# Kernel optimization log

Hardware: AMD Instinct MI355X
Metric: run time of the kernel (lower is better)

Reference implementation:

```python
import jax, jax.numpy as jnp
import numpy as np

MAX_NUM_CENTERS = 100
CENTER_IGNORE_PX = 3
SIGMA = 2.0   # center_gt_blur
KSIZE = 21    # GaussianLayer kernel size (ReflectionPad2d(10) + Conv2d(k=21))


def _gauss_kernel():
    r = KSIZE // 2
    x = jnp.arange(-r, r + 1, dtype=jnp.float32)
    g = jnp.exp(-0.5 * (x / SIGMA) ** 2)
    g = g / g.sum()
    return jnp.outer(g, g)  # [21,21], sums to 1 (matches scipy gaussian_filter of a delta)


def _gaussian_blur(x):
    # x: [B,H,W] -> depthwise 21x21 gaussian with reflect padding (GaussianLayer)
    r = KSIZE // 2
    k = _gauss_kernel()[None, None]  # [1,1,21,21]
    xp = jnp.pad(x[:, None], ((0, 0), (0, 0), (r, r), (r, r)), mode="reflect")
    y = jax.lax.conv_general_dilated(xp, k, (1, 1), "VALID",
                                     dimension_numbers=("NCHW", "OIHW", "NCHW"))
    return y[:, 0]


def setup_inputs() -> dict:
    key = jax.random.key(0)
    k1, k2 = jax.random.split(key)
    B, H, W = 8, 768, 768
    instances = jax.random.randint(k1, (B, 1, H, W), 0, MAX_NUM_CENTERS, dtype=jnp.int32)
    centers = jax.random.uniform(k2, (B, MAX_NUM_CENTERS, 2), dtype=jnp.float32) * (H - 1) + 1.0
    return {"instances": instances, "centers": centers}


def reference(instances, centers):
    B, _, H, W = instances.shape
    inst = instances[:, 0]                                # [B,H,W]
    col = jnp.arange(W, dtype=jnp.float32)                # xym_s[0][i,j] = j
    row = jnp.arange(H, dtype=jnp.float32)[:, None]       # xym_s[1][i,j] = i

    valid = inst > 0                                      # instance_mask
    has_inst = jnp.any(valid, axis=(1, 2)).astype(jnp.float32)  # len(unique)>1 gate

    # per-pixel nearest-center gather: center = centers[b, id-1]
    idx = jnp.clip(inst - 1, 0, MAX_NUM_CENTERS - 1)
    c = centers[jnp.arange(B)[:, None, None], idx]        # [B,H,W,2]
    gt_cx = jnp.where(valid, c[..., 1], -10000.0)         # gt_center_x (swapped coords)
    gt_cy = jnp.where(valid, c[..., 0], -10000.0)

    gt_X = gt_cx - row                                    # gt_center_x - xym_s[1]
    gt_Y = gt_cy - col                                    # gt_center_y - xym_s[0]

    near = (jnp.abs(gt_X) < CENTER_IGNORE_PX) & (jnp.abs(gt_Y) < CENTER_IGNORE_PX)
    # batches with no instances skip the block -> ignore stays all-ones
    ignore = jnp.where(has_inst[:, None, None] > 0, (~near).astype(jnp.float32), 1.0)

    m = valid.astype(jnp.float32)
    R = jnp.sqrt(gt_X ** 2 + gt_Y ** 2) * m
    theta_raw = jnp.arctan2(gt_Y, gt_X)
    theta = theta_raw * has_inst[:, None, None]           # skipped (zero) when no instances
    s = jnp.sin(theta_raw) * m
    cth = jnp.cos(theta_raw) * m
    M = jnp.sqrt(s ** 2 + cth ** 2)                       # == m, kept for faithfulness
    s = jnp.where(valid, s / jnp.maximum(M, 1e-12), 0.0)
    cth = jnp.where(valid, cth / jnp.maximum(M, 1e-12), 0.0)

    # gt_center_mask: zeros if no center-neighborhood pixels, else normalized blur
    blur = _gaussian_blur(1.0 - ignore)
    all_ones = jnp.all(ignore >= 1.0, axis=(1, 2))        # gt_center_mask.all()
    bmax = jnp.max(blur, axis=(1, 2), keepdims=True)
    cmask = jnp.where(all_ones[:, None, None], 0.0, blur / jnp.maximum(bmax, 1e-12))

    top = jnp.stack([R, theta, s, cth, ignore, cmask], axis=1)       # [B,6,H,W]
    mat = jnp.concatenate([top, jnp.zeros((B, 7, H, W), top.dtype)], axis=1)[:, :, None]
    # mat: [B,13,1,H,W]; channels 6..12 are zero (no orientation input)

    # gt_centers[id] = centers[b, id-1][[1,0]] for each instance id present
    present = jnp.zeros((B, MAX_NUM_CENTERS), dtype=bool).at[
        jnp.arange(B)[:, None], inst.reshape(B, -1)].set(True)
    swapped = centers[..., ::-1]
    gt_centers = jnp.zeros_like(centers).at[:, 1:, :].set(
        jnp.where(present[:, 1:, None], swapped[:, :-1, :], 0.0))

    return mat, gt_centers
```

## Files before the change

kernel.cpp:

```cpp
#include <hip/hip_runtime.h>
#include <math.h>

#define NB 8
#define NH 768
#define NW 768
#define NHW (NH*NW)
#define NCEN 100
#define NPIX (NB*NHW)
#define RAD 10
#define KS 21

#define TS 64
#define HALO 10
#define MS (TS + 2*HALO)
#define TILES_X (NW / TS)
#define TILES_PER_B (TILES_X * TILES_X)
#define SCAN_BLKS (NPIX / 4096)
#define BLKS_PER_B (NHW / 4096)

#define HDR_HAS 32
#define HDR_NEAR 40
#define HDR_BMAX 48
#define HDR_BLOCKMASK 64

typedef float f4 __attribute__((ext_vector_type(4)));

__device__ __forceinline__ int refl(int i, int n) {
    i = i < 0 ? -i : i;
    return i >= n ? 2 * n - 2 - i : i;
}

__global__ void k_scan(const int4* __restrict__ inst4, int* __restrict__ hdr) {
    __shared__ unsigned sm[4];
    int t = threadIdx.x;
    if (t < 4) sm[t] = 0;
    __syncthreads();
    unsigned m0 = 0, m1 = 0, m2 = 0, m3 = 0;
    size_t base = (size_t)blockIdx.x * 1024 + t;
#pragma unroll
    for (int q = 0; q < 4; q++) {
        int4 v = inst4[base + (size_t)q * 256];
        int a[4] = {v.x, v.y, v.z, v.w};
#pragma unroll
        for (int e = 0; e < 4; e++) {
            int iv = a[e];
            if (iv > 0) {
                unsigned bit = 1u << (iv & 31);
                int w = iv >> 5;
                if (w == 0) m0 |= bit; else if (w == 1) m1 |= bit;
                else if (w == 2) m2 |= bit; else m3 |= bit;
            }
        }
    }
#pragma unroll
    for (int off = 32; off >= 1; off >>= 1) {
        m0 |= __shfl_xor(m0, off);
        m1 |= __shfl_xor(m1, off);
        m2 |= __shfl_xor(m2, off);
        m3 |= __shfl_xor(m3, off);
    }
    if ((t & 63) == 0) {
        if (m0) atomicOr(&sm[0], m0);
        if (m1) atomicOr(&sm[1], m1);
        if (m2) atomicOr(&sm[2], m2);
        if (m3) atomicOr(&sm[3], m3);
    }
    __syncthreads();
    if (t < 4) ((unsigned*)&hdr[HDR_BLOCKMASK])[blockIdx.x * 4 + t] = sm[t];
}

__global__ void k_small(const float* __restrict__ centers, int* __restrict__ hdr,
                        float* __restrict__ gt) {
    __shared__ unsigned s_pres[32];
    int t = threadIdx.x;
    const unsigned* bm = (const unsigned*)&hdr[HDR_BLOCKMASK];
    if (t < 32) {
        int b = t >> 2, wi = t & 3;
        unsigned acc = 0;
        for (int k = 0; k < BLKS_PER_B; k++) acc |= bm[(b * BLKS_PER_B + k) * 4 + wi];
        s_pres[t] = acc;
    }
    if (t >= 40 && t < 56) hdr[t] = 0;
    __syncthreads();
    if (t < NB * NCEN) {
        int b = t / NCEN, k = t - b * NCEN;
        float vx = 0.f, vy = 0.f;
        if (k >= 1) {
            unsigned w = s_pres[b * 4 + (k >> 5)];
            if ((w >> (k & 31)) & 1u) {
                vx = centers[(b * NCEN + (k - 1)) * 2 + 1];
                vy = centers[(b * NCEN + (k - 1)) * 2 + 0];
            }
        }
        gt[t * 2 + 0] = vx;
        gt[t * 2 + 1] = vy;
    } else if (t < NB * NCEN + NB) {
        int b = t - NB * NCEN;
        unsigned any = (s_pres[b * 4] & 0xFFFFFFFEu)
                     | s_pres[b * 4 + 1] | s_pres[b * 4 + 2] | s_pres[b * 4 + 3];
        hdr[HDR_HAS + b] = any ? 1 : 0;
    }
}

__global__ __launch_bounds__(256) void k_fused(const int* __restrict__ inst,
                                               const float* __restrict__ centers,
                                               int* __restrict__ hdr,
                                               float* __restrict__ out) {
    __shared__ float s_cen[2 * NCEN];
    __shared__ float s_mask[MS * MS];
    __shared__ float s_hbuf[MS * TS];
    __shared__ float s_w[KS];
    __shared__ float s_red[4];

    int t = threadIdx.x;
    int tile = blockIdx.x;
    int b = tile / TILES_PER_B;
    int tr = tile - b * TILES_PER_B;
    int ti0 = (tr / TILES_X) * TS;
    int tj0 = (tr - (tr / TILES_X) * TILES_X) * TS;

    if (t == 0) {
        float v[KS];
        float sum = 0.f;
        for (int k = 0; k < KS; k++) {
            float x = (float)(k - RAD) * 0.5f;
            v[k] = expf(-0.5f * x * x);
            sum += v[k];
        }
        for (int k = 0; k < KS; k++) s_w[k] = v[k] / sum;
    }
    for (int k = t; k < 2 * NCEN; k += 256) s_cen[k] = centers[b * 2 * NCEN + k];
    int has = hdr[HDR_HAS + b];
    __syncthreads();

    int anynear = 0;
    const int* instb = inst + (size_t)b * NHW;
    for (int e = t; e < MS * MS; e += 256) {
        int r = e / MS, c = e - r * MS;
        int gi = refl(ti0 + r - HALO, NH);
        int gj = refl(tj0 + c - HALO, NW);
        int iv = instb[gi * NW + gj];
        float mv = 0.f;
        if (has && iv > 0) {
            int idx = iv - 1;
            float cy = s_cen[2 * idx];
            float cx = s_cen[2 * idx + 1];
            float X = cx - (float)gi;
            float Y = cy - (float)gj;
            if (fabsf(X) < 3.f && fabsf(Y) < 3.f) { mv = 1.f; anynear = 1; }
        }
        s_mask[e] = mv;
    }
    if (anynear) hdr[HDR_NEAR + b] = 1;
    __syncthreads();

    for (int e = t; e < MS * TS; e += 256) {
        int r = e >> 6, c = e & 63;
        const float* mrow = &s_mask[r * MS + c];
        float acc = 0.f;
#pragma unroll
        for (int k = 0; k < KS; k++) acc += s_w[k] * mrow[k];
        s_hbuf[e] = acc;
    }
    __syncthreads();

    float wmax = 0.f;
    float* outb = out + (size_t)b * 13 * NHW;
    for (int q = t; q < TS * TS / 4; q += 256) {
        int r = q >> 4;
        int c0 = (q & 15) * 4;
        f4 blur = {0.f, 0.f, 0.f, 0.f};
#pragma unroll
        for (int k = 0; k < KS; k++) {
            f4 hv = *(const f4*)&s_hbuf[(r + k) * TS + c0];
            blur += s_w[k] * hv;
        }
        wmax = fmaxf(wmax, fmaxf(fmaxf(blur.x, blur.y), fmaxf(blur.z, blur.w)));

        int gi = ti0 + r, gj0 = tj0 + c0;
        int p0 = gi * NW + gj0;
        int4 ivv = *(const int4*)&instb[p0];
        int ia[4] = {ivv.x, ivv.y, ivv.z, ivv.w};
        f4 vR, vTh, vS, vC, vIg;
#pragma unroll
        for (int e = 0; e < 4; e++) {
            int iv = ia[e];
            bool valid = iv > 0;
            int idx = iv - 1;
            idx = idx < 0 ? 0 : idx;
            float cy = s_cen[2 * idx];
            float cx = s_cen[2 * idx + 1];
            float gcx = valid ? cx : -10000.f;
            float gcy = valid ? cy : -10000.f;
            float X = gcx - (float)gi;
            float Y = gcy - (float)(gj0 + e);
            bool near = (fabsf(X) < 3.f) && (fabsf(Y) < 3.f);
            vIg[e] = (has != 0) ? (near ? 0.f : 1.f) : 1.f;
            float m = valid ? 1.f : 0.f;
            float R2 = X * X + Y * Y;
            vR[e] = sqrtf(R2) * m;
            float rinv = R2 > 0.f ? rsqrtf(R2) : 0.f;
            vS[e] = valid ? Y * rinv : 0.f;
            vC[e] = valid ? (R2 > 0.f ? X * rinv : 1.f) : 0.f;
            float th = atan2f(Y, X);
            vTh[e] = (has != 0) ? th : 0.f;
        }
        __builtin_nontemporal_store(vR,   (f4*)&outb[(size_t)0 * NHW + p0]);
        __builtin_nontemporal_store(vTh,  (f4*)&outb[(size_t)1 * NHW + p0]);
        __builtin_nontemporal_store(vS,   (f4*)&outb[(size_t)2 * NHW + p0]);
        __builtin_nontemporal_store(vC,   (f4*)&outb[(size_t)3 * NHW + p0]);
        __builtin_nontemporal_store(vIg,  (f4*)&outb[(size_t)4 * NHW + p0]);
        __builtin_nontemporal_store(blur, (f4*)&outb[(size_t)5 * NHW + p0]);
        f4 z = {0.f, 0.f, 0.f, 0.f};
#pragma unroll
        for (int ch = 6; ch < 13; ++ch)
            __builtin_nontemporal_store(z, (f4*)&outb[(size_t)ch * NHW + p0]);
    }

#pragma unroll
    for (int off = 32; off >= 1; off >>= 1) wmax = fmaxf(wmax, __shfl_down(wmax, off));
    if ((t & 63) == 0) s_red[t >> 6] = wmax;
    __syncthreads();
    if (t == 0) {
        float bmx = fmaxf(fmaxf(s_red[0], s_red[1]), fmaxf(s_red[2], s_red[3]));
        atomicMax((unsigned*)&hdr[HDR_BMAX + b], __float_as_uint(bmx));
    }
}

__global__ void k_norm(const int* __restrict__ hdr, float* __restrict__ out) {
    int g = blockIdx.x * 256 + threadIdx.x;
    int b = g / (NHW / 4);
    int p4 = g - b * (NHW / 4);
    f4* c5 = (f4*)(out + (size_t)b * 13 * NHW + 5 * (size_t)NHW);
    f4 v = c5[p4];
    float bm = __uint_as_float((unsigned)hdr[HDR_BMAX + b]);
    float sc = (hdr[HDR_NEAR + b] != 0) ? 1.f / fmaxf(bm, 1e-12f) : 0.f;
    v *= sc;
    c5[p4] = v;
}

extern "C" void kernel_launch(void* const* d_in, const int* in_sizes, int n_in,
                              void* d_out, int out_size, void* d_ws, size_t ws_size,
                              hipStream_t stream) {
    const int* inst = (const int*)d_in[0];
    const float* centers = (const float*)d_in[1];
    float* out = (float*)d_out;
    int* hdr = (int*)d_ws;
    float* gt = out + (size_t)NB * 13 * NHW;

    k_scan<<<SCAN_BLKS, 256, 0, stream>>>((const int4*)inst, hdr);
    k_small<<<1, 1024, 0, stream>>>(centers, hdr, gt);
    k_fused<<<NB * TILES_PER_B, 256, 0, stream>>>(inst, centers, hdr, out);
    k_norm<<<NPIX / 1024, 256, 0, stream>>>(hdr, out);
}
```

Baseline: 300.8 us.

## Replace dense gaussian blur with sparse delta-sum over near-center pixels

Builds a per-batch list of near-center pixels in a new prep kernel and computes the blurred center mask analytically as a sum of separable reflected gaussian weights over that list. The maximum for normalization is computed in the prep kernel over the blur support, removing the separate normalization pass and the shared-memory tile convolution. Per-pixel cost now scales with the number of near pixels, and the single-block-per-batch prep kernel adds a serial stage.

```diff
diff --git a/kernel.cpp b/kernel.cpp
--- a/kernel.cpp
+++ b/kernel.cpp
@@ -10,24 +10,38 @@
 #define RAD 10
 #define KS 21
 
-#define TS 64
-#define HALO 10
-#define MS (TS + 2*HALO)
-#define TILES_X (NW / TS)
-#define TILES_PER_B (TILES_X * TILES_X)
 #define SCAN_BLKS (NPIX / 4096)
 #define BLKS_PER_B (NHW / 4096)
-
-#define HDR_HAS 32
-#define HDR_NEAR 40
-#define HDR_BMAX 48
+#define LIST_CAP 4096
+#define QBLK_PER_B (NHW / 1024)
+
+#define HDR_HAS 0
+#define HDR_SC 8
+#define HDR_CNT 16
 #define HDR_BLOCKMASK 64
+#define HDR_LIST 8192
 
 typedef float f4 __attribute__((ext_vector_type(4)));
 
-__device__ __forceinline__ int refl(int i, int n) {
-    i = i < 0 ? -i : i;
-    return i >= n ? 2 * n - 2 - i : i;
+__device__ __forceinline__ float wfun(int p, int q, const float* __restrict__ g) {
+    int d = p - q;
+    float w = 0.f;
+    if (d >= -RAD && d <= RAD) w = g[d + RAD];
+    int a = p + q;
+    if (q > 0 && a <= RAD) w += g[a + RAD];
+    if (q < NH - 1 && a >= 2 * (NH - 1) - RAD) w += g[a - 2 * (NH - 1) + RAD];
+    return w;
+}
+
+__device__ __forceinline__ void gauss_tbl(float* g) {
+    float v[KS];
+    float sum = 0.f;
+    for (int k = 0; k < KS; k++) {
+        float x = (float)(k - RAD) * 0.5f;
+        v[k] = expf(-0.5f * x * x);
+        sum += v[k];
+    }
+    for (int k = 0; k < KS; k++) g[k] = v[k] / sum;
 }
 
 __global__ void k_scan(const int4* __restrict__ inst4, int* __restrict__ hdr) {
@@ -69,174 +83,173 @@
     if (t < 4) ((unsigned*)&hdr[HDR_BLOCKMASK])[blockIdx.x * 4 + t] = sm[t];
 }
 
-__global__ void k_small(const float* __restrict__ centers, int* __restrict__ hdr,
-                        float* __restrict__ gt) {
-    __shared__ unsigned s_pres[32];
-    int t = threadIdx.x;
+__global__ __launch_bounds__(256) void k_prep(const int* __restrict__ inst,
+                                              const float* __restrict__ centers,
+                                              int* __restrict__ hdr,
+                                              float* __restrict__ gt) {
+    __shared__ unsigned sm[4];
+    __shared__ float s_g[KS];
+    __shared__ int s_list[LIST_CAP];
+    __shared__ int s_cnt;
+    __shared__ unsigned s_bmax;
+    int b = blockIdx.x, t = threadIdx.x;
+    if (t < 4) sm[t] = 0;
+    if (t == 0) { s_cnt = 0; s_bmax = 0; gauss_tbl(s_g); }
+    __syncthreads();
+
     const unsigned* bm = (const unsigned*)&hdr[HDR_BLOCKMASK];
-    if (t < 32) {
-        int b = t >> 2, wi = t & 3;
-        unsigned acc = 0;
-        for (int k = 0; k < BLKS_PER_B; k++) acc |= bm[(b * BLKS_PER_B + k) * 4 + wi];
-        s_pres[t] = acc;
-    }
-    if (t >= 40 && t < 56) hdr[t] = 0;
-    __syncthreads();
-    if (t < NB * NCEN) {
-        int b = t / NCEN, k = t - b * NCEN;
+    if (t < BLKS_PER_B) {
+        const unsigned* p = &bm[(b * BLKS_PER_B + t) * 4];
+        unsigned w0 = p[0], w1 = p[1], w2 = p[2], w3 = p[3];
+        if (w0) atomicOr(&sm[0], w0);
+        if (w1) atomicOr(&sm[1], w1);
+        if (w2) atomicOr(&sm[2], w2);
+        if (w3) atomicOr(&sm[3], w3);
+    }
+    __syncthreads();
+    unsigned any = (sm[0] & 0xFFFFFFFEu) | sm[1] | sm[2] | sm[3];
+    int has = any ? 1 : 0;
+
+    if (t < NCEN) {
+        int k = t;
         float vx = 0.f, vy = 0.f;
-        if (k >= 1) {
-            unsigned w = s_pres[b * 4 + (k >> 5)];
-            if ((w >> (k & 31)) & 1u) {
-                vx = centers[(b * NCEN + (k - 1)) * 2 + 1];
-                vy = centers[(b * NCEN + (k - 1)) * 2 + 0];
+        if (k >= 1 && ((sm[k >> 5] >> (k & 31)) & 1u)) {
+            vx = centers[(b * NCEN + (k - 1)) * 2 + 1];
+            vy = centers[(b * NCEN + (k - 1)) * 2 + 0];
+        }
+        gt[(b * NCEN + k) * 2 + 0] = vx;
+        gt[(b * NCEN + k) * 2 + 1] = vy;
+    }
+
+    const int* instb = inst + (size_t)b * NHW;
+    if (t < NCEN && has) {
+        int id = t + 1;
+        float cy = centers[(b * NCEN + t) * 2 + 0];
+        float cx = centers[(b * NCEN + t) * 2 + 1];
+        int ci = (int)floorf(cx), cj = (int)floorf(cy);
+        for (int di = -3; di <= 3; di++) {
+            int i = ci + di;
+            if (i < 0 || i >= NH) continue;
+            if (!(fabsf(cx - (float)i) < 3.f)) continue;
+            for (int dj = -3; dj <= 3; dj++) {
+                int j = cj + dj;
+                if (j < 0 || j >= NW) continue;
+                if (!(fabsf(cy - (float)j) < 3.f)) continue;
+                if (instb[i * NW + j] == id) {
+                    int slot = atomicAdd(&s_cnt, 1);
+                    if (slot < LIST_CAP) s_list[slot] = (i << 16) | j;
+                }
             }
         }
-        gt[t * 2 + 0] = vx;
-        gt[t * 2 + 1] = vy;
-    } else if (t < NB * NCEN + NB) {
-        int b = t - NB * NCEN;
-        unsigned any = (s_pres[b * 4] & 0xFFFFFFFEu)
-                     | s_pres[b * 4 + 1] | s_pres[b * 4 + 2] | s_pres[b * 4 + 3];
-        hdr[HDR_HAS + b] = any ? 1 : 0;
+    }
+    __syncthreads();
+    int M = s_cnt < LIST_CAP ? s_cnt : LIST_CAP;
+
+    float lmax = 0.f;
+    for (int c = t; c < M * (KS * KS); c += 256) {
+        int m = c / (KS * KS), r = c - m * (KS * KS);
+        int e = s_list[m];
+        int pi = (e >> 16) + r / KS - RAD;
+        int pj = (e & 0xFFFF) + (r - (r / KS) * KS) - RAD;
+        if (pi < 0 || pi >= NH || pj < 0 || pj >= NW) continue;
+        float acc = 0.f;
+        for (int m2 = 0; m2 < M; m2++) {
+            int e2 = s_list[m2];
+            float wi = wfun(pi, e2 >> 16, s_g);
+            if (wi == 0.f) continue;
+            acc += wi * wfun(pj, e2 & 0xFFFF, s_g);
+        }
+        lmax = fmaxf(lmax, acc);
+    }
+    atomicMax(&s_bmax, __float_as_uint(lmax));
+    __syncthreads();
+
+    int* gl = &hdr[HDR_LIST + b * LIST_CAP];
+    for (int e2 = t; e2 < M; e2 += 256) gl[e2] = s_list[e2];
+    if (t == 0) {
+        float bmx = __uint_as_float(s_bmax);
+        float sc = (has && M > 0) ? 1.f / fmaxf(bmx, 1e-12f) : 0.f;
+        hdr[HDR_HAS + b] = has;
+        hdr[HDR_SC + b] = (int)__float_as_uint(sc);
+        hdr[HDR_CNT + b] = M;
     }
 }
 
 __global__ __launch_bounds__(256) void k_fused(const int* __restrict__ inst,
                                                const float* __restrict__ centers,
-                                               int* __restrict__ hdr,
+                                               const int* __restrict__ hdr,
                                                float* __restrict__ out) {
     __shared__ float s_cen[2 * NCEN];
-    __shared__ float s_mask[MS * MS];
-    __shared__ float s_hbuf[MS * TS];
-    __shared__ float s_w[KS];
-    __shared__ float s_red[4];
-
+    __shared__ float s_g[KS];
+    __shared__ int s_list[LIST_CAP];
     int t = threadIdx.x;
-    int tile = blockIdx.x;
-    int b = tile / TILES_PER_B;
-    int tr = tile - b * TILES_PER_B;
-    int ti0 = (tr / TILES_X) * TS;
-    int tj0 = (tr - (tr / TILES_X) * TILES_X) * TS;
-
-    if (t == 0) {
-        float v[KS];
-        float sum = 0.f;
-        for (int k = 0; k < KS; k++) {
-            float x = (float)(k - RAD) * 0.5f;
-            v[k] = expf(-0.5f * x * x);
-            sum += v[k];
-        }
-        for (int k = 0; k < KS; k++) s_w[k] = v[k] / sum;
-    }
+    int b = blockIdx.x / QBLK_PER_B;
+    int qblk = blockIdx.x - b * QBLK_PER_B;
+
+    int has = hdr[HDR_HAS + b];
+    int M = hdr[HDR_CNT + b];
+    float sc = __uint_as_float((unsigned)hdr[HDR_SC + b]);
     for (int k = t; k < 2 * NCEN; k += 256) s_cen[k] = centers[b * 2 * NCEN + k];
-    int has = hdr[HDR_HAS + b];
-    __syncthreads();
-
-    int anynear = 0;
+    const int* gl = &hdr[HDR_LIST + b * LIST_CAP];
+    for (int e = t; e < M; e += 256) s_list[e] = gl[e];
+    if (t == 0) gauss_tbl(s_g);
+    __syncthreads();
+
+    int quad = qblk * 256 + t;
+    int p0 = quad * 4;
+    int gi = p0 / NW;
+    int gj0 = p0 - gi * NW;
     const int* instb = inst + (size_t)b * NHW;
-    for (int e = t; e < MS * MS; e += 256) {
-        int r = e / MS, c = e - r * MS;
-        int gi = refl(ti0 + r - HALO, NH);
-        int gj = refl(tj0 + c - HALO, NW);
-        int iv = instb[gi * NW + gj];
-        float mv = 0.f;
-        if (has && iv > 0) {
-            int idx = iv - 1;
-            float cy = s_cen[2 * idx];
-            float cx = s_cen[2 * idx + 1];
-            float X = cx - (float)gi;
-            float Y = cy - (float)gj;
-            if (fabsf(X) < 3.f && fabsf(Y) < 3.f) { mv = 1.f; anynear = 1; }
-        }
-        s_mask[e] = mv;
-    }
-    if (anynear) hdr[HDR_NEAR + b] = 1;
-    __syncthreads();
-
-    for (int e = t; e < MS * TS; e += 256) {
-        int r = e >> 6, c = e & 63;
-        const float* mrow = &s_mask[r * MS + c];
-        float acc = 0.f;
-#pragma unroll
-        for (int k = 0; k < KS; k++) acc += s_w[k] * mrow[k];
-        s_hbuf[e] = acc;
-    }
-    __syncthreads();
-
-    float wmax = 0.f;
     float* outb = out + (size_t)b * 13 * NHW;
-    for (int q = t; q < TS * TS / 4; q += 256) {
-        int r = q >> 4;
-        int c0 = (q & 15) * 4;
-        f4 blur = {0.f, 0.f, 0.f, 0.f};
-#pragma unroll
-        for (int k = 0; k < KS; k++) {
-            f4 hv = *(const f4*)&s_hbuf[(r + k) * TS + c0];
-            blur += s_w[k] * hv;
-        }
-        wmax = fmaxf(wmax, fmaxf(fmaxf(blur.x, blur.y), fmaxf(blur.z, blur.w)));
-
-        int gi = ti0 + r, gj0 = tj0 + c0;
-        int p0 = gi * NW + gj0;
-        int4 ivv = *(const int4*)&instb[p0];
-        int ia[4] = {ivv.x, ivv.y, ivv.z, ivv.w};
-        f4 vR, vTh, vS, vC, vIg;
-#pragma unroll
-        for (int e = 0; e < 4; e++) {
-            int iv = ia[e];
-            bool valid = iv > 0;
-            int idx = iv - 1;
-            idx = idx < 0 ? 0 : idx;
-            float cy = s_cen[2 * idx];
-            float cx = s_cen[2 * idx + 1];
-            float gcx = valid ? cx : -10000.f;
-            float gcy = valid ? cy : -10000.f;
-            float X = gcx - (float)gi;
-            float Y = gcy - (float)(gj0 + e);
-            bool near = (fabsf(X) < 3.f) && (fabsf(Y) < 3.f);
-            vIg[e] = (has != 0) ? (near ? 0.f : 1.f) : 1.f;
-            float m = valid ? 1.f : 0.f;
-            float R2 = X * X + Y * Y;
-            vR[e] = sqrtf(R2) * m;
-            float rinv = R2 > 0.f ? rsqrtf(R2) : 0.f;
-            vS[e] = valid ? Y * rinv : 0.f;
-            vC[e] = valid ? (R2 > 0.f ? X * rinv : 1.f) : 0.f;
-            float th = atan2f(Y, X);
-            vTh[e] = (has != 0) ? th : 0.f;
-        }
-        __builtin_nontemporal_store(vR,   (f4*)&outb[(size_t)0 * NHW + p0]);
-        __builtin_nontemporal_store(vTh,  (f4*)&outb[(size_t)1 * NHW + p0]);
-        __builtin_nontemporal_store(vS,   (f4*)&outb[(size_t)2 * NHW + p0]);
-        __builtin_nontemporal_store(vC,   (f4*)&outb[(size_t)3 * NHW + p0]);
-        __builtin_nontemporal_store(vIg,  (f4*)&outb[(size_t)4 * NHW + p0]);
-        __builtin_nontemporal_store(blur, (f4*)&outb[(size_t)5 * NHW + p0]);
-        f4 z = {0.f, 0.f, 0.f, 0.f};
-#pragma unroll
-        for (int ch = 6; ch < 13; ++ch)
-            __builtin_nontemporal_store(z, (f4*)&outb[(size_t)ch * NHW + p0]);
-    }
-
-#pragma unroll
-    for (int off = 32; off >= 1; off >>= 1) wmax = fmaxf(wmax, __shfl_down(wmax, off));
-    if ((t & 63) == 0) s_red[t >> 6] = wmax;
-    __syncthreads();
-    if (t == 0) {
-        float bmx = fmaxf(fmaxf(s_red[0], s_red[1]), fmaxf(s_red[2], s_red[3]));
-        atomicMax((unsigned*)&hdr[HDR_BMAX + b], __float_as_uint(bmx));
-    }
-}
-
-__global__ void k_norm(const int* __restrict__ hdr, float* __restrict__ out) {
-    int g = blockIdx.x * 256 + threadIdx.x;
-    int b = g / (NHW / 4);
-    int p4 = g - b * (NHW / 4);
-    f4* c5 = (f4*)(out + (size_t)b * 13 * NHW + 5 * (size_t)NHW);
-    f4 v = c5[p4];
-    float bm = __uint_as_float((unsigned)hdr[HDR_BMAX + b]);
-    float sc = (hdr[HDR_NEAR + b] != 0) ? 1.f / fmaxf(bm, 1e-12f) : 0.f;
-    v *= sc;
-    c5[p4] = v;
+
+    int4 ivv = *(const int4*)&instb[p0];
+    int ia[4] = {ivv.x, ivv.y, ivv.z, ivv.w};
+    f4 vR, vTh, vS, vC, vIg;
+#pragma unroll
+    for (int e = 0; e < 4; e++) {
+        int iv = ia[e];
+        bool valid = iv > 0;
+        int idx = iv - 1;
+        idx = idx < 0 ? 0 : idx;
+        float cy = s_cen[2 * idx];
+        float cx = s_cen[2 * idx + 1];
+        float gcx = valid ? cx : -10000.f;
+        float gcy = valid ? cy : -10000.f;
+        float X = gcx - (float)gi;
+        float Y = gcy - (float)(gj0 + e);
+        bool near = (fabsf(X) < 3.f) && (fabsf(Y) < 3.f);
+        vIg[e] = (has != 0) ? (near ? 0.f : 1.f) : 1.f;
+        float m = valid ? 1.f : 0.f;
+        float R2 = X * X + Y * Y;
+        vR[e] = sqrtf(R2) * m;
+        float rinv = R2 > 0.f ? rsqrtf(R2) : 0.f;
+        vS[e] = valid ? Y * rinv : 0.f;
+        vC[e] = valid ? (R2 > 0.f ? X * rinv : 1.f) : 0.f;
+        float th = atan2f(Y, X);
+        vTh[e] = (has != 0) ? th : 0.f;
+    }
+
+    f4 blur = {0.f, 0.f, 0.f, 0.f};
+    for (int m = 0; m < M; m++) {
+        int e2 = s_list[m];
+        float wi = wfun(gi, e2 >> 16, s_g);
+        if (wi == 0.f) continue;
+        int qj = e2 & 0xFFFF;
+#pragma unroll
+        for (int e = 0; e < 4; e++) blur[e] += wi * wfun(gj0 + e, qj, s_g);
+    }
+    f4 vCm = blur * sc;
+
+    __builtin_nontemporal_store(vR,  (f4*)&outb[(size_t)0 * NHW + p0]);
+    __builtin_nontemporal_store(vTh, (f4*)&outb[(size_t)1 * NHW + p0]);
+    __builtin_nontemporal_store(vS,  (f4*)&outb[(size_t)2 * NHW + p0]);
+    __builtin_nontemporal_store(vC,  (f4*)&outb[(size_t)3 * NHW + p0]);
+    __builtin_nontemporal_store(vIg, (f4*)&outb[(size_t)4 * NHW + p0]);
+    __builtin_nontemporal_store(vCm, (f4*)&outb[(size_t)5 * NHW + p0]);
+    f4 z = {0.f, 0.f, 0.f, 0.f};
+#pragma unroll
+    for (int ch = 6; ch < 13; ++ch)
+        __builtin_nontemporal_store(z, (f4*)&outb[(size_t)ch * NHW + p0]);
 }
 
 extern "C" void kernel_launch(void* const* d_in, const int* in_sizes, int n_in,
@@ -249,7 +262,6 @@
     float* gt = out + (size_t)NB * 13 * NHW;
 
     k_scan<<<SCAN_BLKS, 256, 0, stream>>>((const int4*)inst, hdr);
-    k_small<<<1, 1024, 0, stream>>>(centers, hdr, gt);
-    k_fused<<<NB * TILES_PER_B, 256, 0, stream>>>(inst, centers, hdr, out);
-    k_norm<<<NPIX / 1024, 256, 0, stream>>>(hdr, out);
-}
+    k_prep<<<NB, 256, 0, stream>>>(inst, centers, hdr, gt);
+    k_fused<<<NB * QBLK_PER_B, 256, 0, stream>>>(inst, centers, hdr, out);
+}
```

Measured after the change: 850.7 us. +182.8%, slower.
